# Performance work log

Measured on AMD Instinct MI355X. Metric: run time of the kernel, lower is better.

## Reference

```python
import jax, jax.numpy as jnp
import numpy as np

B, N, DA, DB = 8, 2048, 768, 1024


def setup_inputs() -> dict:
    key = jax.random.key(0)
    ks = jax.random.split(key, 20)
    s = 0.02
    inp = {
        "x_a": jax.random.normal(ks[0], (B, N, DA), jnp.float32),
        "x_b": jax.random.normal(ks[1], (B, N, DB), jnp.float32),
        # self-attention params (all DB x DB), stored as [in, out]
        "sa_wq": jax.random.normal(ks[2], (DB, DB), jnp.float32) * s,
        "sa_bq": jnp.zeros((DB,), jnp.float32),
        "sa_wk": jax.random.normal(ks[3], (DB, DB), jnp.float32) * s,
        "sa_bk": jnp.zeros((DB,), jnp.float32),
        "sa_wv": jax.random.normal(ks[4], (DB, DB), jnp.float32) * s,
        "sa_bv": jnp.zeros((DB,), jnp.float32),
        "sa_wo": jax.random.normal(ks[5], (DB, DB), jnp.float32) * s,
        "sa_bo": jnp.zeros((DB,), jnp.float32),
        # cross-attention params: q maps DA->DB, rest DB->DB
        "ca_wq": jax.random.normal(ks[6], (DA, DB), jnp.float32) * s,
        "ca_bq": jnp.zeros((DB,), jnp.float32),
        "ca_wk": jax.random.normal(ks[7], (DB, DB), jnp.float32) * s,
        "ca_bk": jnp.zeros((DB,), jnp.float32),
        "ca_wv": jax.random.normal(ks[8], (DB, DB), jnp.float32) * s,
        "ca_bv": jnp.zeros((DB,), jnp.float32),
        "ca_wo": jax.random.normal(ks[9], (DB, DB), jnp.float32) * s,
        "ca_bo": jnp.zeros((DB,), jnp.float32),
    }
    return inp


def _attend(q, k, v, scale):
    # q: [B,Nq,D], k,v: [B,Nk,D]
    scores = jnp.einsum("bqd,bkd->bqk", q, k) / scale
    w = jax.nn.softmax(scores, axis=-1)
    return jnp.einsum("bqk,bkd->bqd", w, v)


def reference(x_a, x_b,
              sa_wq, sa_bq, sa_wk, sa_bk, sa_wv, sa_bv, sa_wo, sa_bo,
              ca_wq, ca_bq, ca_wk, ca_bk, ca_wv, ca_bv, ca_wo, ca_bo):
    # self-attention on x_b; scale = sqrt(embed_dim_b)
    q = x_b @ sa_wq + sa_bq
    k = x_b @ sa_wk + sa_bk
    v = x_b @ sa_wv + sa_bv
    sa_out = _attend(q, k, v, jnp.sqrt(jnp.float32(x_b.shape[-1]))) @ sa_wo + sa_bo
    x_b = x_b + sa_out
    # cross-attention: q from x_a, k/v from updated x_b; scale = sqrt(embed_dim_a)
    q = x_a @ ca_wq + ca_bq
    k = x_b @ ca_wk + ca_bk
    v = x_b @ ca_wv + ca_bv
    ca_out = _attend(q, k, v, jnp.sqrt(jnp.float32(x_a.shape[-1]))) @ ca_wo + ca_bo
    return x_b + ca_out
```

## Files before the change

### kernel.cpp

```cpp
#include <hip/hip_runtime.h>
#include <hip/hip_bf16.h>


#define AS1 __attribute__((address_space(1)))
#define AS3 __attribute__((address_space(3)))

typedef __attribute__((ext_vector_type(8))) short bf16x8;
typedef __attribute__((ext_vector_type(4))) float f32x4;

using bf = __hip_bfloat16;

__global__ __launch_bounds__(512, 1) void gemm256(
    const bf* __restrict__ A, const bf* __restrict__ BT,
    const float* __restrict__ bias, const float* __restrict__ biasB,
    const float* __restrict__ biasC,
    const float* __restrict__ resid32, const bf* __restrict__ resid16,
    bf* __restrict__ C16, bf* __restrict__ C16b, bf* __restrict__ C16c,
    float* __restrict__ C32,
    int M, int Nc, int K, float alpha,
    long sA, long sB, long sC, int tstore, int nseg)
{
    __shared__ __align__(16) char lds[131072];

    const int tid  = threadIdx.x;
    const int wave = tid >> 6;
    const int lane = tid & 63;
    const int wm = wave >> 2;
    const int wn = wave & 3;
    const int m0 = blockIdx.y * 256;
    const int n0 = blockIdx.x * 256;
    const long zC = (long)blockIdx.z * sC;
    A  += (long)blockIdx.z * sA;
    BT += (long)blockIdx.z * sB;

    const int fl = lane & 15, qd = lane >> 4;
    const int sr = lane >> 3;
    const int scn = (lane & 7) ^ sr;
    const long ldb = (long)K * 2;

    const char* gA = (const char*)A  + (long)(m0 + wave * 16 + sr) * ldb + scn * 16;
    const char* gB = (const char*)BT + (long)(n0 + wave * 16 + sr) * ldb + scn * 16;

    auto stage_ht = [&](int s) {
        const int t = s >> 2, r = s & 3;
        const char* g = ((r & 1) ? gB : gA) + (long)((r >> 1) * 128) * ldb + (long)t * 128;
        char* l = lds + ((t & 1) * 65536) + r * 16384 + wave * 2048;
        __builtin_amdgcn_global_load_lds((const AS1 void*)g,               (AS3 void*)l,          16, 0, 0);
        __builtin_amdgcn_global_load_lds((const AS1 void*)(g + 8 * ldb),   (AS3 void*)(l + 1024), 16, 0, 0);
    };

    const int xo = fl & 7;
    const int so0 = ((0 | qd) ^ xo) * 16;
    const int so1 = ((4 | qd) ^ xo) * 16;
    const char* Abase = lds + (wm ? 2 : 0) * 16384 + fl * 128;
    const char* Bbase = lds + ((wn >> 1) ? 3 : 1) * 16384 + (wn & 1) * 64 * 128 + fl * 128;

    f32x4 acc[8][4];
#pragma unroll
    for (int i = 0; i < 8; ++i)
#pragma unroll
        for (int j = 0; j < 4; ++j)
            acc[i][j] = (f32x4){0.f, 0.f, 0.f, 0.f};

    bf16x8 afr[2][4][2];
    bf16x8 bfr[2][2][2];

#define READ_A(mq, SL) { const char* pA_ = Abase + (SL) * 65536 + (mq) * 8192; \
    _Pragma("unroll") for (int f_ = 0; f_ < 4; ++f_) { \
        afr[mq][f_][0] = *(const bf16x8*)(pA_ + f_ * 2048 + so0); \
        afr[mq][f_][1] = *(const bf16x8*)(pA_ + f_ * 2048 + so1); } }

#define READ_B(nq, SL) { const char* pB_ = Bbase + (SL) * 65536 + (nq) * 4096; \
    _Pragma("unroll") for (int g_ = 0; g_ < 2; ++g_) { \
        bfr[nq][g_][0] = *(const bf16x8*)(pB_ + g_ * 2048 + so0); \
        bfr[nq][g_][1] = *(const bf16x8*)(pB_ + g_ * 2048 + so1); } }

#define MFMA_Q(mq, nq) { \
    __builtin_amdgcn_s_setprio(1); \
    _Pragma("unroll") for (int f_ = 0; f_ < 4; ++f_) \
    _Pragma("unroll") for (int g_ = 0; g_ < 2; ++g_) { \
        acc[(mq)*4+f_][(nq)*2+g_] = __builtin_amdgcn_mfma_f32_16x16x32_bf16( \
            afr[mq][f_][0], bfr[nq][g_][0], acc[(mq)*4+f_][(nq)*2+g_], 0, 0, 0); \
        acc[(mq)*4+f_][(nq)*2+g_] = __builtin_amdgcn_mfma_f32_16x16x32_bf16( \
            afr[mq][f_][1], bfr[nq][g_][1], acc[(mq)*4+f_][(nq)*2+g_], 0, 0, 0); } \
    __builtin_amdgcn_s_setprio(0); }

#define BAR() __builtin_amdgcn_s_barrier()
#define VMCNT4() asm volatile("s_waitcnt vmcnt(4)" ::: "memory")
#define VMCNT0() asm volatile("s_waitcnt vmcnt(0)" ::: "memory")
#define STG(S) { if ((S) < nht) stage_ht(S); }

    const int NT    = K >> 6;
    const int niter = NT >> 1;
    const int nht   = NT << 2;

#pragma unroll
    for (int s = 0; s < 6; ++s) stage_ht(s);
    VMCNT4();
    BAR();

    for (int I = 0; I < niter; ++I) {
        const int s0 = 8 * I + 6;
        const bool last = (I == niter - 1);
        READ_A(0, 0); READ_B(0, 0); STG(s0 + 0); BAR(); MFMA_Q(0, 0); BAR();
        READ_A(1, 0); READ_B(1, 0); STG(s0 + 1); BAR(); MFMA_Q(1, 1); BAR();
        STG(s0 + 2); BAR(); MFMA_Q(0, 1); BAR();
        STG(s0 + 3); BAR(); MFMA_Q(1, 0);
        if (last) { VMCNT0(); } else { VMCNT4(); }
        BAR();
        READ_A(0, 1); READ_B(0, 1); STG(s0 + 4); BAR(); MFMA_Q(0, 0); BAR();
        READ_A(1, 1); READ_B(1, 1); STG(s0 + 5); BAR(); MFMA_Q(1, 1); BAR();
        STG(s0 + 6); BAR(); MFMA_Q(0, 1); BAR();
        STG(s0 + 7); BAR(); MFMA_Q(1, 0);
        if (!last) { VMCNT4(); }
        BAR();
    }

    if (nseg == 1) {
        const long ldc = Nc;
#pragma unroll
        for (int i = 0; i < 8; ++i) {
#pragma unroll
            for (int j = 0; j < 4; ++j) {
#pragma unroll
                for (int r = 0; r < 4; ++r) {
                    const int row = m0 + wm * 128 + i * 16 + qd * 4 + r;
                    const int col = n0 + wn * 64 + j * 16 + fl;
                    float v = acc[i][j][r] * alpha;
                    if (bias) v += bias[col];
                    if (tstore & 1) {
                        const long idx = (long)(row >> 11) * ((long)Nc * 2048)
                                       + (long)col * 2048 + (row & 2047);
                        C16[idx] = __float2bfloat16(v);
                    } else {
                        const long idx = zC + (long)row * ldc + col;
                        if (resid32) v += resid32[idx];
                        if (resid16) v += __bfloat162float(resid16[idx]);
                        if (C16) C16[idx] = __float2bfloat16(v);
                        if (C32) C32[idx] = v;
                    }
                }
            }
        }
    } else {
        const int seg = n0 >> 10;
        bf* dst = (seg == 0) ? C16 : ((seg == 1) ? C16b : C16c);
        const float* bseg = (seg == 0) ? bias : ((seg == 1) ? biasB : biasC);
        const int trans = (tstore >> seg) & 1;
        const int cb = n0 & 1023;
#pragma unroll
        for (int i = 0; i < 8; ++i) {
#pragma unroll
            for (int j = 0; j < 4; ++j) {
#pragma unroll
                for (int r = 0; r < 4; ++r) {
                    const int row = m0 + wm * 128 + i * 16 + qd * 4 + r;
                    const int col = cb + wn * 64 + j * 16 + fl;
                    float v = acc[i][j][r] * alpha + bseg[col];
                    const long idx = trans
                        ? (long)(row >> 11) * (1024L * 2048) + (long)col * 2048 + (row & 2047)
                        : (long)row * 1024 + col;
                    dst[idx] = __float2bfloat16(v);
                }
            }
        }
    }
#undef READ_A
#undef READ_B
#undef MFMA_Q
#undef BAR
#undef VMCNT4
#undef VMCNT0
#undef STG
}

__global__ __launch_bounds__(256) void cast_f32_bf16(
    const float* __restrict__ in, bf* __restrict__ out, long n)
{
    long i = ((long)blockIdx.x * 256 + threadIdx.x) * 8;
    if (i >= n) return;
    float4 a = *(const float4*)(in + i);
    float4 b = *(const float4*)(in + i + 4);
    bf o[8] = {__float2bfloat16(a.x), __float2bfloat16(a.y),
               __float2bfloat16(a.z), __float2bfloat16(a.w),
               __float2bfloat16(b.x), __float2bfloat16(b.y),
               __float2bfloat16(b.z), __float2bfloat16(b.w)};
    *(bf16x8*)(out + i) = *(bf16x8*)o;
}

__global__ __launch_bounds__(256) void transpose_f32_bf16(
    const float* __restrict__ in, bf* __restrict__ out, int R, int C)
{
    __shared__ bf t[32][33];
    const int c0 = blockIdx.x * 32, r0 = blockIdx.y * 32;
    const int tx = threadIdx.x, ty = threadIdx.y;
#pragma unroll
    for (int i = ty; i < 32; i += 8)
        t[i][tx] = __float2bfloat16(in[(long)(r0 + i) * C + c0 + tx]);
    __syncthreads();
#pragma unroll
    for (int i = ty; i < 32; i += 8)
        out[(long)(c0 + i) * R + r0 + tx] = t[tx][i];
}

__global__ __launch_bounds__(256) void softmax_rows(bf* __restrict__ S)
{
    const long row = blockIdx.x;
    bf* p = S + row * 2048;
    const int tx = threadIdx.x;

    float v[8];
    float m = -3.0e38f;
#pragma unroll
    for (int i = 0; i < 8; i++) {
        v[i] = __bfloat162float(p[tx + 256 * i]);
        m = fmaxf(m, v[i]);
    }
    __shared__ float red[4];
#pragma unroll
    for (int o = 1; o < 64; o <<= 1) m = fmaxf(m, __shfl_xor(m, o, 64));
    if ((tx & 63) == 0) red[tx >> 6] = m;
    __syncthreads();
    m = fmaxf(fmaxf(red[0], red[1]), fmaxf(red[2], red[3]));

    float s = 0.f;
#pragma unroll
    for (int i = 0; i < 8; i++) { v[i] = __expf(v[i] - m); s += v[i]; }
#pragma unroll
    for (int o = 1; o < 64; o <<= 1) s += __shfl_xor(s, o, 64);
    __syncthreads();
    if ((tx & 63) == 0) red[tx >> 6] = s;
    __syncthreads();
    const float inv = 1.0f / (red[0] + red[1] + red[2] + red[3]);
#pragma unroll
    for (int i = 0; i < 8; i++) p[tx + 256 * i] = __float2bfloat16(v[i] * inv);
}

extern "C" void kernel_launch(void* const* d_in, const int* in_sizes, int n_in,
                              void* d_out, int out_size, void* d_ws, size_t ws_size,
                              hipStream_t stream)
{
    const int Bb = 8, Nn = 2048, DA = 768, DB = 1024;
    const long Mt = (long)Bb * Nn;

    const float* x_a   = (const float*)d_in[0];
    const float* x_b   = (const float*)d_in[1];
    const float* sa_wq = (const float*)d_in[2];  const float* sa_bq = (const float*)d_in[3];
    const float* sa_wk = (const float*)d_in[4];  const float* sa_bk = (const float*)d_in[5];
    const float* sa_wv = (const float*)d_in[6];  const float* sa_bv = (const float*)d_in[7];
    const float* sa_wo = (const float*)d_in[8];  const float* sa_bo = (const float*)d_in[9];
    const float* ca_wq = (const float*)d_in[10]; const float* ca_bq = (const float*)d_in[11];
    const float* ca_wk = (const float*)d_in[12]; const float* ca_bk = (const float*)d_in[13];
    const float* ca_wv = (const float*)d_in[14]; const float* ca_bv = (const float*)d_in[15];
    const float* ca_wo = (const float*)d_in[16]; const float* ca_bo = (const float*)d_in[17];
    float* out = (float*)d_out;
    (void)in_sizes; (void)n_in; (void)out_size; (void)ws_size;

    char* ws = (char*)d_ws;
    size_t off = 0;
    auto alloc = [&](size_t bytes) -> bf* {
        bf* p = (bf*)(ws + off);
        off += (bytes + 255) & ~(size_t)255;
        return p;
    };
    bf* wqkvT = alloc((size_t)3 * DB * DB * 2);
    bf* woT   = alloc((size_t)DB * DB * 2);
    bf* cwqT  = alloc((size_t)DB * DA * 2);
    bf* ckvT  = alloc((size_t)2 * DB * DB * 2);
    bf* cwoT  = alloc((size_t)DB * DB * 2);
    bf* slA   = alloc((size_t)Mt * DB * 2);
    bf* slQ   = alloc((size_t)Mt * DB * 2);
    bf* slK   = alloc((size_t)Mt * DB * 2);
    bf* slV   = alloc((size_t)Mt * DB * 2);
    bf* S     = alloc((size_t)Bb * Nn * Nn * 2);

    const dim3 tb(32, 8);
    const dim3 blk(256);
    const dim3 blk5(512);
    const long sQ = (long)Nn * DB;
    const long sS = (long)Nn * Nn;
    const float* nf = nullptr;
    const bf*    nb = nullptr;
    bf*          no = nullptr;

    transpose_f32_bf16<<<dim3(DB/32, DB/32), tb, 0, stream>>>(sa_wq, wqkvT,                 DB, DB);
    transpose_f32_bf16<<<dim3(DB/32, DB/32), tb, 0, stream>>>(sa_wk, wqkvT + (size_t)DB*DB, DB, DB);
    transpose_f32_bf16<<<dim3(DB/32, DB/32), tb, 0, stream>>>(sa_wv, wqkvT + (size_t)2*DB*DB, DB, DB);
    transpose_f32_bf16<<<dim3(DB/32, DB/32), tb, 0, stream>>>(sa_wo, woT,  DB, DB);
    transpose_f32_bf16<<<dim3(DB/32, DA/32), tb, 0, stream>>>(ca_wq, cwqT, DA, DB);
    transpose_f32_bf16<<<dim3(DB/32, DB/32), tb, 0, stream>>>(ca_wk, ckvT,                 DB, DB);
    transpose_f32_bf16<<<dim3(DB/32, DB/32), tb, 0, stream>>>(ca_wv, ckvT + (size_t)DB*DB, DB, DB);
    transpose_f32_bf16<<<dim3(DB/32, DB/32), tb, 0, stream>>>(ca_wo, cwoT, DB, DB);

    cast_f32_bf16<<<dim3((unsigned)(Mt * DB / 8 / 256)), blk, 0, stream>>>(x_b, slA, Mt * DB);
    gemm256<<<dim3(3*DB/256, Mt/256, 1), blk5, 0, stream>>>(
        slA, wqkvT, sa_bq, sa_bk, sa_bv, nf, nb, slQ, slK, slV, nullptr,
        (int)Mt, 3*DB, DB, 1.0f, 0, 0, 0, 0b100, 3);
    gemm256<<<dim3(Nn/256, Nn/256, Bb), blk5, 0, stream>>>(
        slQ, slK, nf, nf, nf, nf, nb, S, no, no, nullptr,
        Nn, Nn, DB, 0.03125f, sQ, sQ, sS, 0, 1);
    softmax_rows<<<dim3((unsigned)(Bb * Nn)), blk, 0, stream>>>(S);
    gemm256<<<dim3(DB/256, Nn/256, Bb), blk5, 0, stream>>>(
        S, slV, nf, nf, nf, nf, nb, slK, no, no, nullptr,
        Nn, DB, Nn, 1.0f, sS, sQ, sQ, 0, 1);
    gemm256<<<dim3(DB/256, Mt/256, 1), blk5, 0, stream>>>(
        slK, woT, sa_bo, nf, nf, x_b, nb, slQ, no, no, nullptr,
        (int)Mt, DB, DB, 1.0f, 0, 0, 0, 0, 1);

    cast_f32_bf16<<<dim3((unsigned)(Mt * DA / 8 / 256)), blk, 0, stream>>>(x_a, slA, Mt * DA);
    gemm256<<<dim3(DB/256, Mt/256, 1), blk5, 0, stream>>>(
        slA, cwqT, ca_bq, nf, nf, nf, nb, slK, no, no, nullptr,
        (int)Mt, DB, DA, 1.0f, 0, 0, 0, 0, 1);
    gemm256<<<dim3(2*DB/256, Mt/256, 1), blk5, 0, stream>>>(
        slQ, ckvT, ca_bk, ca_bv, nf, nf, nb, slV, slA, no, nullptr,
        (int)Mt, 2*DB, DB, 1.0f, 0, 0, 0, 0b10, 2);
    gemm256<<<dim3(Nn/256, Nn/256, Bb), blk5, 0, stream>>>(
        slK, slV, nf, nf, nf, nf, nb, S, no, no, nullptr,
        Nn, Nn, DB, 0.036084391824351615f, sQ, sQ, sS, 0, 1);
    softmax_rows<<<dim3((unsigned)(Bb * Nn)), blk, 0, stream>>>(S);
    gemm256<<<dim3(DB/256, Nn/256, Bb), blk5, 0, stream>>>(
        S, slA, nf, nf, nf, nf, nb, slV, no, no, nullptr,
        Nn, DB, Nn, 1.0f, sS, sQ, sQ, 0, 1);
    gemm256<<<dim3(DB/256, Mt/256, 1), blk5, 0, stream>>>(
        slV, cwoT, ca_bo, nf, nf, nf, slQ, no, no, no, out,
        (int)Mt, DB, DB, 1.0f, 0, 0, 0, 0, 1);
}
```

Baseline: 1.135 ms.

## Deepen GEMM prefetch, hoist LDS fragment reads, add sched barriers and XCD-aware tile remap

The bf16 GEMM now issues seven half-tile stages ahead instead of six, waits with vmcnt(6), and reads all A/B fragments for a k-slice at the start of each half-iteration instead of interleaving the reads with the MFMA quarters. Barriers are wrapped in sched_barrier so the compiler cannot move work across them. Workgroup IDs are remapped so that consecutive tiles land on the same XCD when the tile count is a multiple of 8, which is meant to improve L2 reuse. The changes aim to hide more global-load latency and cut cache misses. The cost is more register pressure from holding every fragment at once, and the stage schedule becomes more fragile.

```diff
diff --git a/kernel.cpp b/kernel.cpp
--- a/kernel.cpp
+++ b/kernel.cpp
@@ -27,8 +27,14 @@
     const int lane = tid & 63;
     const int wm = wave >> 2;
     const int wn = wave & 3;
-    const int m0 = blockIdx.y * 256;
-    const int n0 = blockIdx.x * 256;
+
+    const int gx = gridDim.x, gy = gridDim.y;
+    int wg = blockIdx.y * gx + blockIdx.x;
+    const int nwg = gx * gy;
+    if (!(nwg & 7)) wg = (wg & 7) * (nwg >> 3) + (wg >> 3);
+    const int m0 = (wg / gx) * 256;
+    const int n0 = (wg % gx) * 256;
+
     const long zC = (long)blockIdx.z * sC;
     A  += (long)blockIdx.z * sA;
     BT += (long)blockIdx.z * sB;
@@ -85,8 +91,9 @@
             afr[mq][f_][1], bfr[nq][g_][1], acc[(mq)*4+f_][(nq)*2+g_], 0, 0, 0); } \
     __builtin_amdgcn_s_setprio(0); }
 
-#define BAR() __builtin_amdgcn_s_barrier()
-#define VMCNT4() asm volatile("s_waitcnt vmcnt(4)" ::: "memory")
+#define SB()  __builtin_amdgcn_sched_barrier(0)
+#define BARS() { SB(); __builtin_amdgcn_s_barrier(); SB(); }
+#define VMCNT6() asm volatile("s_waitcnt vmcnt(6)" ::: "memory")
 #define VMCNT0() asm volatile("s_waitcnt vmcnt(0)" ::: "memory")
 #define STG(S) { if ((S) < nht) stage_ht(S); }
 
@@ -95,25 +102,27 @@
     const int nht   = NT << 2;
 
 #pragma unroll
-    for (int s = 0; s < 6; ++s) stage_ht(s);
-    VMCNT4();
-    BAR();
+    for (int s = 0; s < 7; ++s) stage_ht(s);
+    VMCNT6();
+    BARS();
 
     for (int I = 0; I < niter; ++I) {
-        const int s0 = 8 * I + 6;
+        const int s0 = 8 * I + 7;
         const bool last = (I == niter - 1);
-        READ_A(0, 0); READ_B(0, 0); STG(s0 + 0); BAR(); MFMA_Q(0, 0); BAR();
-        READ_A(1, 0); READ_B(1, 0); STG(s0 + 1); BAR(); MFMA_Q(1, 1); BAR();
-        STG(s0 + 2); BAR(); MFMA_Q(0, 1); BAR();
-        STG(s0 + 3); BAR(); MFMA_Q(1, 0);
-        if (last) { VMCNT0(); } else { VMCNT4(); }
-        BAR();
-        READ_A(0, 1); READ_B(0, 1); STG(s0 + 4); BAR(); MFMA_Q(0, 0); BAR();
-        READ_A(1, 1); READ_B(1, 1); STG(s0 + 5); BAR(); MFMA_Q(1, 1); BAR();
-        STG(s0 + 6); BAR(); MFMA_Q(0, 1); BAR();
-        STG(s0 + 7); BAR(); MFMA_Q(1, 0);
-        if (!last) { VMCNT4(); }
-        BAR();
+        READ_A(0, 0); READ_B(0, 0); READ_A(1, 0); READ_B(1, 0);
+        STG(s0 + 0); BARS(); MFMA_Q(0, 0); BARS();
+        STG(s0 + 1); BARS(); MFMA_Q(1, 1); BARS();
+        STG(s0 + 2); BARS(); MFMA_Q(0, 1); BARS();
+        STG(s0 + 3); BARS(); MFMA_Q(1, 0);
+        if (last) { VMCNT0(); } else { VMCNT6(); }
+        BARS();
+        READ_A(0, 1); READ_B(0, 1); READ_A(1, 1); READ_B(1, 1);
+        STG(s0 + 4); BARS(); MFMA_Q(0, 0); BARS();
+        STG(s0 + 5); BARS(); MFMA_Q(1, 1); BARS();
+        STG(s0 + 6); BARS(); MFMA_Q(0, 1); BARS();
+        STG(s0 + 7); BARS(); MFMA_Q(1, 0);
+        if (!last) { VMCNT6(); }
+        BARS();
     }
 
     if (nseg == 1) {
@@ -168,8 +177,9 @@
 #undef READ_A
 #undef READ_B
 #undef MFMA_Q
-#undef BAR
-#undef VMCNT4
+#undef SB
+#undef BARS
+#undef VMCNT6
 #undef VMCNT0
 #undef STG
 }
```

New measurement: 1.147 ms. No clear change (+1.0%).

## Restructure GEMM main loop schedule and add XCD-aware workgroup remapping

Applied to the files above, without the earlier changes.

Reworks the 256x256 bf16 GEMM's K-loop into an eight-phase schedule. A-fragment reads are double-buffered across phases, B fragments are kept in separate registers, and each stage issues loads for one matrix half-tile, so LDS reads and global-to-LDS copies overlap MFMA work more evenly. It also remaps workgroup IDs in groups of 8 so that neighbouring tiles land on the same XCD for L2 reuse. The costs are more fragment registers and a more intricate barrier and vmcnt protocol, which could hurt correctness or occupancy.

```diff
diff --git a/kernel.cpp b/kernel.cpp
--- a/kernel.cpp
+++ b/kernel.cpp
@@ -27,33 +27,39 @@
     const int lane = tid & 63;
     const int wm = wave >> 2;
     const int wn = wave & 3;
-    const int m0 = blockIdx.y * 256;
-    const int n0 = blockIdx.x * 256;
+
+    const int gx = gridDim.x, gy = gridDim.y;
+    int wg = blockIdx.y * gx + blockIdx.x;
+    const int nwg = gx * gy;
+    if (!(nwg & 7)) wg = (wg & 7) * (nwg >> 3) + (wg >> 3);
+    const int m0 = (wg / gx) * 256;
+    const int n0 = (wg % gx) * 256;
+
     const long zC = (long)blockIdx.z * sC;
     A  += (long)blockIdx.z * sA;
     BT += (long)blockIdx.z * sB;
 
     const int fl = lane & 15, qd = lane >> 4;
-    const int sr = lane >> 3;
-    const int scn = (lane & 7) ^ sr;
     const long ldb = (long)K * 2;
 
-    const char* gA = (const char*)A  + (long)(m0 + wave * 16 + sr) * ldb + scn * 16;
-    const char* gB = (const char*)BT + (long)(n0 + wave * 16 + sr) * ldb + scn * 16;
-
-    auto stage_ht = [&](int s) {
-        const int t = s >> 2, r = s & 3;
-        const char* g = ((r & 1) ? gB : gA) + (long)((r >> 1) * 128) * ldb + (long)t * 128;
-        char* l = lds + ((t & 1) * 65536) + r * 16384 + wave * 2048;
-        __builtin_amdgcn_global_load_lds((const AS1 void*)g,               (AS3 void*)l,          16, 0, 0);
-        __builtin_amdgcn_global_load_lds((const AS1 void*)(g + 8 * ldb),   (AS3 void*)(l + 1024), 16, 0, 0);
+    const int scn = (lane & 7) ^ (lane >> 3);
+    const char* gA = (const char*)A  + (long)(m0 + (lane >> 3)) * ldb + scn * 16;
+    const char* gB = (const char*)BT + (long)(n0 + (lane >> 3)) * ldb + scn * 16;
+
+    auto stage = [&](int mat, int h, int t) {
+        const char* g = (mat ? gB : gA) + (long)(h * 128 + wave * 8) * ldb + (long)t * 128;
+        char* l = lds + (t & 1) * 65536 + mat * 32768 + h * 16384 + wave * 1024;
+        __builtin_amdgcn_global_load_lds((const AS1 void*)g,            (AS3 void*)l,        16, 0, 0);
+        __builtin_amdgcn_global_load_lds((const AS1 void*)(g + 64*ldb), (AS3 void*)(l + 8192), 16, 0, 0);
     };
 
-    const int xo = fl & 7;
-    const int so0 = ((0 | qd) ^ xo) * 16;
-    const int so1 = ((4 | qd) ^ xo) * 16;
-    const char* Abase = lds + (wm ? 2 : 0) * 16384 + fl * 128;
-    const char* Bbase = lds + ((wn >> 1) ? 3 : 1) * 16384 + (wn & 1) * 64 * 128 + fl * 128;
+    const int s0slot = qd ^ (fl & 7);
+    const int so0 = s0slot * 16;
+    const int so1 = (s0slot ^ 4) * 16;
+    const char* AbH0 = lds + wm * 16384 + fl * 128 + so0;
+    const char* AbH1 = lds + wm * 16384 + fl * 128 + so1;
+    const char* BbH0 = lds + 32768 + (wn >> 1) * 16384 + (wn & 1) * 8192 + fl * 128 + so0;
+    const char* BbH1 = lds + 32768 + (wn >> 1) * 16384 + (wn & 1) * 8192 + fl * 128 + so1;
 
     f32x4 acc[8][4];
 #pragma unroll
@@ -62,58 +68,70 @@
         for (int j = 0; j < 4; ++j)
             acc[i][j] = (f32x4){0.f, 0.f, 0.f, 0.f};
 
-    bf16x8 afr[2][4][2];
-    bf16x8 bfr[2][2][2];
-
-#define READ_A(mq, SL) { const char* pA_ = Abase + (SL) * 65536 + (mq) * 8192; \
+    bf16x8 aA[4][2], aB[4][2];
+    bf16x8 bP[2][2], bN[2][2], bQ1[2][2];
+
+#define RD_A(dst, SL, mq) { \
+    const char* pa0_ = AbH0 + (SL) * 65536 + (mq) * 8192; \
+    const char* pa1_ = AbH1 + (SL) * 65536 + (mq) * 8192; \
     _Pragma("unroll") for (int f_ = 0; f_ < 4; ++f_) { \
-        afr[mq][f_][0] = *(const bf16x8*)(pA_ + f_ * 2048 + so0); \
-        afr[mq][f_][1] = *(const bf16x8*)(pA_ + f_ * 2048 + so1); } }
-
-#define READ_B(nq, SL) { const char* pB_ = Bbase + (SL) * 65536 + (nq) * 4096; \
+        dst[f_][0] = *(const bf16x8*)(pa0_ + f_ * 2048); \
+        dst[f_][1] = *(const bf16x8*)(pa1_ + f_ * 2048); } }
+
+#define RD_B(dst, SL, nq) { \
+    const char* pb0_ = BbH0 + (SL) * 65536 + (nq) * 4096; \
+    const char* pb1_ = BbH1 + (SL) * 65536 + (nq) * 4096; \
     _Pragma("unroll") for (int g_ = 0; g_ < 2; ++g_) { \
-        bfr[nq][g_][0] = *(const bf16x8*)(pB_ + g_ * 2048 + so0); \
-        bfr[nq][g_][1] = *(const bf16x8*)(pB_ + g_ * 2048 + so1); } }
-
-#define MFMA_Q(mq, nq) { \
+        dst[g_][0] = *(const bf16x8*)(pb0_ + g_ * 2048); \
+        dst[g_][1] = *(const bf16x8*)(pb1_ + g_ * 2048); } }
+
+#define MFMA_Q(AF, BF, mq, nq) { \
     __builtin_amdgcn_s_setprio(1); \
     _Pragma("unroll") for (int f_ = 0; f_ < 4; ++f_) \
-    _Pragma("unroll") for (int g_ = 0; g_ < 2; ++g_) { \
+    _Pragma("unroll") for (int g_ = 0; g_ < 2; ++g_) \
+    _Pragma("unroll") for (int h_ = 0; h_ < 2; ++h_) \
         acc[(mq)*4+f_][(nq)*2+g_] = __builtin_amdgcn_mfma_f32_16x16x32_bf16( \
-            afr[mq][f_][0], bfr[nq][g_][0], acc[(mq)*4+f_][(nq)*2+g_], 0, 0, 0); \
-        acc[(mq)*4+f_][(nq)*2+g_] = __builtin_amdgcn_mfma_f32_16x16x32_bf16( \
-            afr[mq][f_][1], bfr[nq][g_][1], acc[(mq)*4+f_][(nq)*2+g_], 0, 0, 0); } \
+            AF[f_][h_], BF[g_][h_], acc[(mq)*4+f_][(nq)*2+g_], 0, 0, 0); \
     __builtin_amdgcn_s_setprio(0); }
 
 #define BAR() __builtin_amdgcn_s_barrier()
-#define VMCNT4() asm volatile("s_waitcnt vmcnt(4)" ::: "memory")
-#define VMCNT0() asm volatile("s_waitcnt vmcnt(0)" ::: "memory")
-#define STG(S) { if ((S) < nht) stage_ht(S); }
+#define VMC(N) asm volatile("s_waitcnt vmcnt(" #N ")" ::: "memory")
 
     const int NT    = K >> 6;
     const int niter = NT >> 1;
-    const int nht   = NT << 2;
-
-#pragma unroll
-    for (int s = 0; s < 6; ++s) stage_ht(s);
-    VMCNT4();
+
+#pragma unroll
+    for (int t = 0; t < 2; ++t) {
+        stage(0, 0, t); stage(1, 0, t); stage(0, 1, t); stage(1, 1, t);
+    }
+    VMC(6);
     BAR();
+    RD_A(aA, 0, 0);
 
     for (int I = 0; I < niter; ++I) {
-        const int s0 = 8 * I + 6;
-        const bool last = (I == niter - 1);
-        READ_A(0, 0); READ_B(0, 0); STG(s0 + 0); BAR(); MFMA_Q(0, 0); BAR();
-        READ_A(1, 0); READ_B(1, 0); STG(s0 + 1); BAR(); MFMA_Q(1, 1); BAR();
-        STG(s0 + 2); BAR(); MFMA_Q(0, 1); BAR();
-        STG(s0 + 3); BAR(); MFMA_Q(1, 0);
-        if (last) { VMCNT0(); } else { VMCNT4(); }
-        BAR();
-        READ_A(0, 1); READ_B(0, 1); STG(s0 + 4); BAR(); MFMA_Q(0, 0); BAR();
-        READ_A(1, 1); READ_B(1, 1); STG(s0 + 5); BAR(); MFMA_Q(1, 1); BAR();
-        STG(s0 + 6); BAR(); MFMA_Q(0, 1); BAR();
-        STG(s0 + 7); BAR(); MFMA_Q(1, 0);
-        if (!last) { VMCNT4(); }
-        BAR();
+        const int t2a = 2 * I + 2, t2b = 2 * I + 3;
+        const bool sa = t2a < NT;
+        RD_B(bP, 0, 0); RD_B(bQ1, 0, 1);
+        if (sa) stage(0, 0, t2a);
+        BAR(); MFMA_Q(aA, bP, 0, 0); BAR();
+        RD_A(aB, 0, 1);
+        if (sa) stage(1, 0, t2a);
+        BAR(); MFMA_Q(aA, bQ1, 0, 1); BAR();
+        RD_A(aA, 1, 0);
+        if (sa) stage(0, 1, t2a);
+        BAR(); MFMA_Q(aB, bQ1, 1, 1); BAR();
+        if (sa) { stage(1, 1, t2a); VMC(6); } else { VMC(0); }
+        BAR(); MFMA_Q(aB, bP, 1, 0); BAR();
+        RD_B(bN, 1, 0); RD_B(bQ1, 1, 1);
+        if (sa) stage(0, 0, t2b);
+        BAR(); MFMA_Q(aA, bN, 0, 0); BAR();
+        RD_A(aB, 1, 1);
+        if (sa) stage(1, 0, t2b);
+        BAR(); MFMA_Q(aA, bQ1, 0, 1); BAR();
+        if (sa) { RD_A(aA, 0, 0); stage(0, 1, t2b); }
+        BAR(); MFMA_Q(aB, bQ1, 1, 1); BAR();
+        if (sa) { stage(1, 1, t2b); VMC(6); }
+        BAR(); MFMA_Q(aB, bN, 1, 0); BAR();
     }
 
     if (nseg == 1) {
@@ -165,13 +183,11 @@
             }
         }
     }
-#undef READ_A
-#undef READ_B
+#undef RD_A
+#undef RD_B
 #undef MFMA_Q
 #undef BAR
-#undef VMCNT4
-#undef VMCNT0
-#undef STG
+#undef VMC
 }
 
 __global__ __launch_bounds__(256) void cast_f32_bf16(
```

Measured after the change: 1.109 ms. 1.02x faster.
